# Kernel tuning notes

Measured on AMD Instinct MI355X. Metric: run time of the kernel, lower is better.

Reference implementation:

```python
import jax, jax.numpy as jnp
import numpy as np

EPS = 1e-4
TAU = 0.1
GAMMA = 64.0
RADIUS = 1.0
N_HEADS = 4
N_SPLIT = 4


def _l2norm(x, axis=-1):
    return x / jnp.maximum(jnp.linalg.norm(x, axis=axis, keepdims=True), 1e-12)


def _pd2(a, b):
    # pairwise squared distances: (B,N,M)
    return (jnp.sum(a * a, -1)[:, :, None] + jnp.sum(b * b, -1)[:, None, :]
            - 2.0 * jnp.einsum('bnd,bmd->bnm', a, b))


def _sim_matrix(xyz, nf, radius, gamma):
    # radius-masked Gaussian feature affinity, zero diagonal
    N = xyz.shape[1]
    d2x = _pd2(xyz, xyz)
    d2f = _pd2(nf, nf)
    A = jnp.exp(-gamma * d2f / nf.shape[-1]) * (d2x < radius * radius).astype(nf.dtype)
    return A * (1.0 - jnp.eye(N, dtype=A.dtype))


def _norm_lap(A, eps):
    deg = A.sum(-1)
    dinv = jax.lax.rsqrt(deg + eps)
    na = A * dinv[:, :, None] * dinv[:, None, :]
    lap = jnp.eye(A.shape[1], dtype=A.dtype) - na
    return lap, na


def _mincut(X, na, W1, b1, W2, b2, tau):
    # one GCN layer + temperature softmax soft assignment; pooled = weighted mean
    h = jax.nn.relu(jnp.einsum('bnm,bmc->bnc', na, X) @ W1 + b1)
    s = jax.nn.softmax((h @ W2 + b2) / tau, axis=-1)  # (B,N,K)
    denom = s.sum(1)[:, :, None] + EPS                # (B,K,1)
    c_fea = jnp.einsum('bnk,bnc->bkc', s, X) / denom
    return c_fea, s


def _centers(xyz, s):
    denom = s.sum(1)[:, :, None] + EPS
    return jnp.einsum('bnk,bnd->bkd', s, xyz) / denom


def _assignment_loss(p_xyz, c_xyz, s):
    d2 = _pd2(p_xyz, c_xyz)
    return jnp.mean(jnp.sum(s * d2, -1))


def _welsch(p_xyz, c_xyz, sigma):
    d2min = jnp.min(_pd2(p_xyz, c_xyz), -1)
    return jnp.mean(1.0 - jnp.exp(-d2min / (2.0 * sigma * sigma)))


def _knn_affinity(xyz, k):
    N = xyz.shape[1]
    d2 = _pd2(xyz, xyz)
    eye = jnp.eye(N, dtype=d2.dtype)
    neg = -(d2 + 1e6 * eye)
    thresh = jax.lax.top_k(neg, k)[0][..., -1:]
    mask = (neg >= thresh).astype(d2.dtype)
    A = jnp.exp(-d2) * mask * (1.0 - eye)
    return jnp.maximum(A, jnp.swapaxes(A, 1, 2))


def _cut_loss(na, xyz, alpha):
    N = xyz.shape[1]
    lap = jnp.eye(N, dtype=na.dtype) - na
    quad = jnp.einsum('bnd,bnm,bmd->b', xyz, lap, xyz)
    return alpha * jnp.mean(quad / N)


def _cross_attn(gf, cf, Wq, Wk, Wv, Wo, n_heads):
    B, N, C = gf.shape
    M = cf.shape[1]
    dh = C // n_heads
    q = (gf @ Wq).reshape(B, N, n_heads, dh)
    k = (cf @ Wk).reshape(B, M, n_heads, dh)
    v = (cf @ Wv).reshape(B, M, n_heads, dh)
    scores = jnp.einsum('bnhd,bmhd->bhnm', q, k) / np.sqrt(dh).astype(np.float32)
    attn = jax.nn.softmax(scores, -1)
    out = jnp.einsum('bhnm,bmhd->bnhd', attn, v).reshape(B, N, C) @ Wo
    return out, attn.mean(1)


def setup_inputs() -> dict:
    key = jax.random.key(0)
    ks = jax.random.split(key, 20)
    B, N_sp, C, H, K = 2, 1024, 256, 128, 64
    Kg = K // N_SPLIT
    sc = 1.0 / np.sqrt(C)
    sh = 1.0 / np.sqrt(H)
    return {
        'g_fea': jax.random.normal(ks[0], (B, N_sp, C), jnp.float32),
        'g_xyz': jax.random.uniform(ks[1], (B, N_sp, 3), jnp.float32),
        'p_fea_0': jax.random.normal(ks[2], (B, 4096, C), jnp.float32),
        'p_xyz_0': jax.random.uniform(ks[3], (B, 4096, 3), jnp.float32),
        'p_fea_1': jax.random.normal(ks[4], (B, 2048, C), jnp.float32),
        'p_xyz_1': jax.random.uniform(ks[5], (B, 2048, 3), jnp.float32),
        'lW1': jax.random.normal(ks[6], (C, H), jnp.float32) * sc,
        'lb1': jnp.zeros((H,), jnp.float32),
        'lW2': jax.random.normal(ks[7], (H, K), jnp.float32) * sh,
        'lb2': jnp.zeros((K,), jnp.float32),
        'gW1': jax.random.normal(ks[8], (C, H), jnp.float32) * sc,
        'gb1': jnp.zeros((H,), jnp.float32),
        'gW2': jax.random.normal(ks[9], (H, Kg), jnp.float32) * sh,
        'gb2': jnp.zeros((Kg,), jnp.float32),
        'Wq': jax.random.normal(ks[10], (C, C), jnp.float32) * sc,
        'Wk': jax.random.normal(ks[11], (C, C), jnp.float32) * sc,
        'Wv': jax.random.normal(ks[12], (C, C), jnp.float32) * sc,
        'Wo': jax.random.normal(ks[13], (C, C), jnp.float32) * sc,
    }


def reference(g_fea, g_xyz, p_fea_0, p_xyz_0, p_fea_1, p_xyz_1,
              lW1, lb1, lW2, lb2, gW1, gb1, gW2, gb2, Wq, Wk, Wv, Wo):
    l_loss = jnp.zeros((), jnp.float32)
    cx_list, cf_list = [], []
    for p_xyz_i, p_fea_i in ((p_xyz_0, p_fea_0), (p_xyz_1, p_fea_1)):
        nf = _l2norm(p_fea_i)
        A = _sim_matrix(p_xyz_i, nf, RADIUS, GAMMA)
        na = _norm_lap(A, EPS)[1]
        c_fea_i, s_i = _mincut(p_fea_i, na, lW1, lb1, lW2, lb2, TAU)
        c_xyz_i = _centers(p_xyz_i, s_i)
        c2p = jnp.einsum('bnk,bkc->bnc', s_i, jax.lax.stop_gradient(c_fea_i))
        l_loss = l_loss + _assignment_loss(p_xyz_i, c_xyz_i, s_i)
        l_loss = l_loss + jnp.linalg.norm(_l2norm(c2p) - nf) + _welsch(p_xyz_i, c_xyz_i, 1.0)
        cx_list.append(c_xyz_i)
        cf_list.append(c_fea_i)
    c_xyz = jnp.concatenate(cx_list, 1)
    c_fea = jnp.concatenate(cf_list, 1)
    A_c = _knn_affinity(c_xyz, 2 * N_SPLIT)
    na_c = _norm_lap(A_c, EPS)[1]
    c_fea_g, gs = _mincut(c_fea, na_c, gW1, gb1, gW2, gb2, TAU)
    c_xyz_g = _centers(c_xyz, gs)
    cut_loss_c = _assignment_loss(c_xyz, c_xyz_g, gs)
    agg, G_t = _cross_attn(g_fea, c_fea_g, Wq, Wk, Wv, Wo, N_HEADS)
    A_g = _sim_matrix(g_xyz, _l2norm(g_fea), 4.0 * RADIUS, GAMMA)
    ass_loss = _cut_loss(_norm_lap(A_g, EPS)[1], g_xyz, 1e-4)
    g_loss = jnp.mean(jnp.sum(jnp.linalg.norm(_l2norm(agg) - _l2norm(g_fea), axis=-1), 1)) + ass_loss
    return agg, l_loss + cut_loss_c, g_loss
```

## Files before the change

### kernel.cpp

```cpp
#include <hip/hip_runtime.h>

#define EPSF 1e-4f

typedef __attribute__((ext_vector_type(8))) short bf16x8;
typedef __attribute__((ext_vector_type(4))) float f32x4;

__device__ __forceinline__ unsigned short f2bf(float f){
    unsigned int u = __float_as_uint(f);
    return (unsigned short)((u + 0x7FFF + ((u >> 16) & 1)) >> 16);
}
__device__ __forceinline__ float bf2f(unsigned short u){
    return __uint_as_float(((unsigned int)u) << 16);
}
__device__ __forceinline__ float waveSum(float v){
    #pragma unroll
    for (int o = 32; o; o >>= 1) v += __shfl_xor(v, o, 64);
    return v;
}
__device__ __forceinline__ float waveMin(float v){
    #pragma unroll
    for (int o = 32; o; o >>= 1) v = fminf(v, __shfl_xor(v, o, 64));
    return v;
}
__device__ __forceinline__ float waveMax(float v){
    #pragma unroll
    for (int o = 32; o; o >>= 1) v = fmaxf(v, __shfl_xor(v, o, 64));
    return v;
}
__device__ __forceinline__ float blockReduceSum(float v, float* red, int nthr){
    int t = threadIdx.x;
    red[t] = v; __syncthreads();
    for (int s = nthr >> 1; s > 0; s >>= 1){
        if (t < s) red[t] += red[t + s];
        __syncthreads();
    }
    float r = red[0]; __syncthreads();
    return r;
}

__global__ void l2norm_kernel(const float* __restrict__ x, float* __restrict__ outf,
                              unsigned short* __restrict__ outb, int rows){
    __shared__ float red[256];
    int row = blockIdx.x, t = threadIdx.x;
    float v = x[(long)row*256 + t];
    float s = blockReduceSum(v*v, red, 256);
    float nrm = fmaxf(sqrtf(s), 1e-12f);
    float r = v / nrm;
    outf[(long)row*256 + t] = r;
    outb[(long)row*256 + t] = f2bf(r);
}

__global__ void cvt_bf16_kernel(const float* __restrict__ in, unsigned short* __restrict__ out, long n4){
    long i = (long)blockIdx.x*256 + threadIdx.x;
    if (i < n4){
        float4 v = ((const float4*)in)[i];
        unsigned int lo = f2bf(v.x) | ((unsigned int)f2bf(v.y) << 16);
        unsigned int hi = f2bf(v.z) | ((unsigned int)f2bf(v.w) << 16);
        uint2 u; u.x = lo; u.y = hi;
        ((uint2*)out)[i] = u;
    }
}

__global__ void tcvt_kernel(const float* __restrict__ W, unsigned short* __restrict__ WT,
                            int Rw, int Cw){
    __shared__ float tile[64][65];
    int r0 = blockIdx.x*64, c0 = blockIdx.y*64;
    int t = threadIdx.x;
    for (int idx = t; idx < 4096; idx += 256){
        int rr = idx >> 6, cc = idx & 63;
        tile[rr][cc] = (r0+rr < Rw && c0+cc < Cw) ? W[(long)(r0+rr)*Cw + c0+cc] : 0.f;
    }
    __syncthreads();
    for (int idx = t; idx < 4096; idx += 256){
        int cc = idx >> 6, rr = idx & 63;
        if (r0+rr < Rw && c0+cc < Cw)
            WT[(long)(c0+cc)*Rw + r0+rr] = f2bf(tile[rr][cc]);
    }
}

__global__ __launch_bounds__(256) void gram_mfma_kernel(const unsigned short* __restrict__ nf,
                                                        const float* __restrict__ xyz,
                                                        unsigned short* __restrict__ A,
                                                        float* __restrict__ deg,
                                                        int N, float r2, float scale){
    __shared__ short tA[128*32], tB[128*32];
    __shared__ float xa[384], xb[384];
    int tid = threadIdx.x;
    int n0 = blockIdx.y*128, m0 = blockIdx.x*128;
    for (int i = tid; i < 384; i += 256){ xa[i] = xyz[n0*3 + i]; xb[i] = xyz[m0*3 + i]; }
    int w = tid >> 6, l = tid & 63;
    int wy = w >> 1, wx = w & 1;
    int lg = l >> 4, lr = l & 15;
    int srow = tid >> 2, sc = tid & 3;
    f32x4 zero = {0.f, 0.f, 0.f, 0.f};
    f32x4 acc[4][4];
    #pragma unroll
    for (int i = 0; i < 4; ++i)
        #pragma unroll
        for (int j = 0; j < 4; ++j) acc[i][j] = zero;
    for (int kt = 0; kt < 256; kt += 32){
        __syncthreads();
        #pragma unroll
        for (int p = 0; p < 2; ++p){
            int row = srow + p*64;
            uint4 va = *(const uint4*)(nf + (long)(n0+row)*256 + kt + sc*8);
            uint4 vb = *(const uint4*)(nf + (long)(m0+row)*256 + kt + sc*8);
            *(uint4*)(tA + row*32 + sc*8) = va;
            *(uint4*)(tB + row*32 + sc*8) = vb;
        }
        __syncthreads();
        bf16x8 af[4], bfr[4];
        #pragma unroll
        for (int f = 0; f < 4; ++f){
            af[f]  = *(const bf16x8*)(tA + (wy*64 + f*16 + lr)*32 + lg*8);
            bfr[f] = *(const bf16x8*)(tB + (wx*64 + f*16 + lr)*32 + lg*8);
        }
        #pragma unroll
        for (int i = 0; i < 4; ++i)
            #pragma unroll
            for (int j = 0; j < 4; ++j)
                acc[i][j] = __builtin_amdgcn_mfma_f32_16x16x32_bf16(af[i], bfr[j], acc[i][j], 0, 0, 0);
    }
    #pragma unroll
    for (int fi = 0; fi < 4; ++fi){
        #pragma unroll
        for (int r = 0; r < 4; ++r){
            int n_ = wy*64 + fi*16 + lg*4 + r;
            int gn = n0 + n_;
            float rowacc = 0.f;
            #pragma unroll
            for (int fj = 0; fj < 4; ++fj){
                int m_ = wx*64 + fj*16 + lr;
                float dx = xa[n_*3+0]-xb[m_*3+0];
                float dy = xa[n_*3+1]-xb[m_*3+1];
                float dz = xa[n_*3+2]-xb[m_*3+2];
                float d2x = dx*dx + dy*dy + dz*dz;
                int gm = m0 + m_;
                float dot = acc[fi][fj][r];
                float val = (d2x < r2 && gn != gm) ? expf(scale*(2.f*dot - 2.f)) : 0.f;
                A[(long)gn*N + gm] = f2bf(val);
                rowacc += val;
            }
            rowacc += __shfl_xor(rowacc, 1, 64);
            rowacc += __shfl_xor(rowacc, 2, 64);
            rowacc += __shfl_xor(rowacc, 4, 64);
            rowacc += __shfl_xor(rowacc, 8, 64);
            if (lr == 0) atomicAdd(&deg[gn], rowacc);
        }
    }
}

__global__ __launch_bounds__(256) void transpose_scale_kernel(const float* __restrict__ fea,
                                                              const float* __restrict__ deg,
                                                              unsigned short* __restrict__ feaT,
                                                              unsigned short* __restrict__ xsT, int N){
    __shared__ float tile[64][65];
    __shared__ float dl[64];
    int m0 = blockIdx.x*64, c0 = blockIdx.y*64;
    int t = threadIdx.x;
    int lr = t >> 2, lc = (t & 3)*16;
    #pragma unroll
    for (int j = 0; j < 4; ++j){
        float4 v = *(const float4*)(fea + (long)(m0+lr)*256 + c0 + lc + j*4);
        tile[lr][lc+j*4+0] = v.x; tile[lr][lc+j*4+1] = v.y;
        tile[lr][lc+j*4+2] = v.z; tile[lr][lc+j*4+3] = v.w;
    }
    if (t < 64) dl[t] = rsqrtf(deg[m0+t] + EPSF);
    __syncthreads();
    unsigned short vr[16] __attribute__((aligned(16)));
    unsigned short vs[16] __attribute__((aligned(16)));
    #pragma unroll
    for (int j = 0; j < 16; ++j){
        float raw = tile[lc+j][lr];
        vr[j] = f2bf(raw);
        vs[j] = f2bf(raw * dl[lc+j]);
    }
    long off = (long)(c0+lr)*N + m0 + lc;
    *(uint4*)(feaT + off)     = *(uint4*)&vr[0];
    *(uint4*)(feaT + off + 8) = *(uint4*)&vr[8];
    *(uint4*)(xsT + off)      = *(uint4*)&vs[0];
    *(uint4*)(xsT + off + 8)  = *(uint4*)&vs[8];
}

__global__ __launch_bounds__(256) void ax_mfma_kernel(const unsigned short* __restrict__ A,
                                                      const unsigned short* __restrict__ xsT,
                                                      float* __restrict__ PY, int N){
    __shared__ short tA[128*32], tB[128*32];
    int tid = threadIdx.x;
    int c0 = blockIdx.x*128, n0 = blockIdx.y*128;
    int half = blockIdx.z;
    int kbase = half*(N/2), kend = kbase + N/2;
    int w = tid >> 6, l = tid & 63;
    int wy = w >> 1, wx = w & 1;
    int lg = l >> 4, lr = l & 15;
    int srow = tid >> 2, sc = tid & 3;
    f32x4 zero = {0.f, 0.f, 0.f, 0.f};
    f32x4 acc[4][4];
    #pragma unroll
    for (int i = 0; i < 4; ++i)
        #pragma unroll
        for (int j = 0; j < 4; ++j) acc[i][j] = zero;
    for (int kt = kbase; kt < kend; kt += 32){
        __syncthreads();
        #pragma unroll
        for (int p = 0; p < 2; ++p){
            int row = srow + p*64;
            uint4 va = *(const uint4*)(A   + (long)(n0+row)*N + kt + sc*8);
            uint4 vb = *(const uint4*)(xsT + (long)(c0+row)*N + kt + sc*8);
            *(uint4*)(tA + row*32 + sc*8) = va;
            *(uint4*)(tB + row*32 + sc*8) = vb;
        }
        __syncthreads();
        bf16x8 af[4], bfr[4];
        #pragma unroll
        for (int f = 0; f < 4; ++f){
            af[f]  = *(const bf16x8*)(tA + (wy*64 + f*16 + lr)*32 + lg*8);
            bfr[f] = *(const bf16x8*)(tB + (wx*64 + f*16 + lr)*32 + lg*8);
        }
        #pragma unroll
        for (int i = 0; i < 4; ++i)
            #pragma unroll
            for (int j = 0; j < 4; ++j)
                acc[i][j] = __builtin_amdgcn_mfma_f32_16x16x32_bf16(af[i], bfr[j], acc[i][j], 0, 0, 0);
    }
    float* out = PY + (long)half*N*256;
    #pragma unroll
    for (int fi = 0; fi < 4; ++fi){
        #pragma unroll
        for (int fj = 0; fj < 4; ++fj){
            #pragma unroll
            for (int r = 0; r < 4; ++r){
                int n_ = n0 + wy*64 + fi*16 + lg*4 + r;
                int c_ = c0 + wx*64 + fj*16 + lr;
                out[(long)n_*256 + c_] = acc[fi][fj][r];
            }
        }
    }
}

__global__ void combine_kernel(const float* __restrict__ PY, const float* __restrict__ deg,
                               unsigned short* __restrict__ Yb, int N){
    long i = (long)blockIdx.x*256 + threadIdx.x;
    long e = i*8;
    const float4* p0 = (const float4*)(PY + e);
    const float4* p1 = (const float4*)(PY + (long)N*256 + e);
    float4 a0 = p0[0], a1 = p0[1], b0 = p1[0], b1 = p1[1];
    float d = rsqrtf(deg[e >> 8] + EPSF);
    unsigned short vb[8] __attribute__((aligned(16)));
    vb[0] = f2bf((a0.x+b0.x)*d); vb[1] = f2bf((a0.y+b0.y)*d);
    vb[2] = f2bf((a0.z+b0.z)*d); vb[3] = f2bf((a0.w+b0.w)*d);
    vb[4] = f2bf((a1.x+b1.x)*d); vb[5] = f2bf((a1.y+b1.y)*d);
    vb[6] = f2bf((a1.z+b1.z)*d); vb[7] = f2bf((a1.w+b1.w)*d);
    *(uint4*)(Yb + e) = *(uint4*)vb;
}

__global__ __launch_bounds__(256) void gemm_XW_mfma_kernel(const unsigned short* __restrict__ X,
                                                           const unsigned short* __restrict__ WT,
                                                           const float* __restrict__ bias,
                                                           float* __restrict__ outF,
                                                           unsigned short* __restrict__ outB,
                                                           int R, int Ci, int Co, int relu){
    __shared__ short tA[128*32], tB[128*32];
    int tid = threadIdx.x;
    int c0 = blockIdx.x*128, r0 = blockIdx.y*128;
    int w = tid >> 6, l = tid & 63;
    int wy = w >> 1, wx = w & 1;
    int lg = l >> 4, lr = l & 15;
    int srow = tid >> 2, sc = tid & 3;
    f32x4 zero = {0.f, 0.f, 0.f, 0.f};
    f32x4 acc[4][4];
    #pragma unroll
    for (int i = 0; i < 4; ++i)
        #pragma unroll
        for (int j = 0; j < 4; ++j) acc[i][j] = zero;
    for (int kt = 0; kt < Ci; kt += 32){
        __syncthreads();
        #pragma unroll
        for (int p = 0; p < 2; ++p){
            int row = srow + p*64;
            uint4 va = {0,0,0,0}, vb = {0,0,0,0};
            int ar = r0 + row, br = c0 + row;
            if (ar < R)  va = *(const uint4*)(X  + (long)ar*Ci + kt + sc*8);
            if (br < Co) vb = *(const uint4*)(WT + (long)br*Ci + kt + sc*8);
            *(uint4*)(tA + row*32 + sc*8) = va;
            *(uint4*)(tB + row*32 + sc*8) = vb;
        }
        __syncthreads();
        bf16x8 af[4], bfr[4];
        #pragma unroll
        for (int f = 0; f < 4; ++f){
            af[f]  = *(const bf16x8*)(tA + (wy*64 + f*16 + lr)*32 + lg*8);
            bfr[f] = *(const bf16x8*)(tB + (wx*64 + f*16 + lr)*32 + lg*8);
        }
        #pragma unroll
        for (int i = 0; i < 4; ++i)
            #pragma unroll
            for (int j = 0; j < 4; ++j)
                acc[i][j] = __builtin_amdgcn_mfma_f32_16x16x32_bf16(af[i], bfr[j], acc[i][j], 0, 0, 0);
    }
    #pragma unroll
    for (int fi = 0; fi < 4; ++fi){
        #pragma unroll
        for (int fj = 0; fj < 4; ++fj){
            #pragma unroll
            for (int r = 0; r < 4; ++r){
                int rr = r0 + wy*64 + fi*16 + lg*4 + r;
                int cc = c0 + wx*64 + fj*16 + lr;
                if (rr < R && cc < Co){
                    float v = acc[fi][fj][r] + (bias ? bias[cc] : 0.f);
                    if (relu) v = fmaxf(v, 0.f);
                    if (outF) outF[(long)rr*Co + cc] = v;
                    if (outB) outB[(long)rr*Co + cc] = f2bf(v);
                }
            }
        }
    }
}

__global__ __launch_bounds__(256) void gemm_splitk_kernel(const float* __restrict__ X,
                                                          const float* __restrict__ W0,
                                                          const float* __restrict__ W1,
                                                          float* __restrict__ part,
                                                          int R, int Ci, int Co, int Ks){
    __shared__ float sa[32][65], sb[32][65];
    int tid = threadIdx.x, tx = tid & 15, ty = tid >> 4;
    int c0 = blockIdx.x * 64, r0 = blockIdx.y * 64;
    int z = blockIdx.z;
    const float* W = (z / Ks) ? W1 : W0;
    int kchunk = Ci / Ks, kst = (z % Ks) * kchunk;
    float acc[4][4] = {};
    for (int kt = kst; kt < kst + kchunk; kt += 32){
        #pragma unroll
        for (int p = 0; p < 8; ++p){
            int idx = p*256 + tid;
            int k = idx & 31, i = idx >> 5;
            int rr = r0 + i;
            sa[k][i] = (rr < R) ? X[(long)rr*Ci + kt + k] : 0.f;
            int j = idx & 63, kk = idx >> 6;
            int cc = c0 + j;
            sb[kk][j] = (cc < Co) ? W[(long)(kt+kk)*Co + cc] : 0.f;
        }
        __syncthreads();
        #pragma unroll
        for (int k = 0; k < 32; ++k){
            float a0=sa[k][ty*4+0],a1=sa[k][ty*4+1],a2=sa[k][ty*4+2],a3=sa[k][ty*4+3];
            float b0=sb[k][tx*4+0],b1=sb[k][tx*4+1],b2=sb[k][tx*4+2],b3=sb[k][tx*4+3];
            acc[0][0]+=a0*b0; acc[0][1]+=a0*b1; acc[0][2]+=a0*b2; acc[0][3]+=a0*b3;
            acc[1][0]+=a1*b0; acc[1][1]+=a1*b1; acc[1][2]+=a1*b2; acc[1][3]+=a1*b3;
            acc[2][0]+=a2*b0; acc[2][1]+=a2*b1; acc[2][2]+=a2*b2; acc[2][3]+=a2*b3;
            acc[3][0]+=a3*b0; acc[3][1]+=a3*b1; acc[3][2]+=a3*b2; acc[3][3]+=a3*b3;
        }
        __syncthreads();
    }
    float* outp = part + (long)z*R*Co;
    #pragma unroll
    for (int r = 0; r < 4; ++r){
        #pragma unroll
        for (int c = 0; c < 4; ++c){
            int rr = r0 + ty*4 + r, cc = c0 + tx*4 + c;
            if (rr < R && cc < Co) outp[(long)rr*Co + cc] = acc[r][c];
        }
    }
}

__global__ void combine_bias_kernel(const float* __restrict__ part, const float* __restrict__ bias,
                                    float* __restrict__ out, int R, int Co, int Ks, int relu){
    long i = (long)blockIdx.x*256 + threadIdx.x;
    if (i < (long)R*Co){
        long zs = (long)R*Co;
        float s = 0.f;
        for (int q = 0; q < Ks; ++q) s += part[q*zs + i];
        float v = s + (bias ? bias[i % Co] : 0.f);
        if (relu) v = fmaxf(v, 0.f);
        out[i] = v;
    }
}

__global__ __launch_bounds__(256) void softmaxT_kernel(float* __restrict__ s,
                                                       unsigned short* __restrict__ sT,
                                                       int sStride, float invtau){
    __shared__ unsigned short st[64][65];
    int blk = blockIdx.x, t = threadIdx.x, w = t >> 6, l = t & 63;
    #pragma unroll
    for (int i = 0; i < 16; ++i){
        int rloc = w + 4*i;
        long row = (long)blk*64 + rloc;
        float v = s[row*64 + l] * invtau;
        float mx = waveMax(v);
        float e = expf(v - mx);
        float sum = waveSum(e);
        float p = e / sum;
        s[row*64 + l] = p;
        st[l][rloc] = f2bf(p);
    }
    __syncthreads();
    int k = t >> 2, j = (t & 3)*16;
    unsigned short vbuf[16] __attribute__((aligned(16)));
    #pragma unroll
    for (int q = 0; q < 16; ++q) vbuf[q] = st[k][j+q];
    long off = (long)k*sStride + (long)blk*64 + j;
    *(uint4*)(sT + off)     = *(uint4*)&vbuf[0];
    *(uint4*)(sT + off + 8) = *(uint4*)&vbuf[8];
}

__global__ __launch_bounds__(256) void stx_mfma_kernel(const unsigned short* __restrict__ sT,
                                                       const unsigned short* __restrict__ feaT,
                                                       float* __restrict__ part,
                                                       int N, int split, int sStride){
    __shared__ short tA[64*32], tB[256*32];
    int tid = threadIdx.x;
    int z = blockIdx.x, b = z / split, chunk = z % split;
    int L = N / split, kst = chunk * L;
    const unsigned short* sTb = sT + (long)b*N;
    const unsigned short* fT  = feaT + (long)b*256*N;
    int w = tid >> 6, l = tid & 63;
    int lg = l >> 4, lr = l & 15;
    f32x4 zero = {0.f, 0.f, 0.f, 0.f};
    f32x4 acc[4][4];
    #pragma unroll
    for (int i = 0; i < 4; ++i)
        #pragma unroll
        for (int j = 0; j < 4; ++j) acc[i][j] = zero;
    int srow = tid >> 2, koff = (tid & 3)*8;
    for (int kt = kst; kt < kst + L; kt += 32){
        __syncthreads();
        *(uint4*)(tA + srow*32 + koff) = *(const uint4*)(sTb + (long)srow*sStride + kt + koff);
        #pragma unroll
        for (int p = 0; p < 4; ++p){
            int row = srow + p*64;
            *(uint4*)(tB + row*32 + koff) = *(const uint4*)(fT + (long)row*N + kt + koff);
        }
        __syncthreads();
        bf16x8 af[4], bfr[4];
        #pragma unroll
        for (int f = 0; f < 4; ++f){
            af[f]  = *(const bf16x8*)(tA + (f*16 + lr)*32 + lg*8);
            bfr[f] = *(const bf16x8*)(tB + (w*64 + f*16 + lr)*32 + lg*8);
        }
        #pragma unroll
        for (int i = 0; i < 4; ++i)
            #pragma unroll
            for (int j = 0; j < 4; ++j)
                acc[i][j] = __builtin_amdgcn_mfma_f32_16x16x32_bf16(af[i], bfr[j], acc[i][j], 0, 0, 0);
    }
    float* outp = part + (long)z*64*256;
    #pragma unroll
    for (int fi = 0; fi < 4; ++fi){
        #pragma unroll
        for (int fj = 0; fj < 4; ++fj){
            #pragma unroll
            for (int r = 0; r < 4; ++r){
                int kc = fi*16 + lg*4 + r;
                int cc = w*64 + fj*16 + lr;
                outp[(long)kc*256 + cc] = acc[fi][fj][r];
            }
        }
    }
}

__global__ void softmax_kernel(float* __restrict__ x, int Kc, float tau){
    int row = blockIdx.x, lane = threadIdx.x;
    bool act = lane < Kc;
    float v = act ? x[(long)row*Kc + lane] / tau : -1e30f;
    float mx = v;
    #pragma unroll
    for (int o = 32; o; o >>= 1) mx = fmaxf(mx, __shfl_xor(mx, o, 64));
    float e = act ? expf(v - mx) : 0.f;
    float s = e;
    #pragma unroll
    for (int o = 32; o; o >>= 1) s += __shfl_xor(s, o, 64);
    if (act) x[(long)row*Kc + lane] = e / s;
}

__global__ void cluster_xyz_kernel(const float* __restrict__ s, const float* __restrict__ xyz,
                                   float* __restrict__ outx, float* __restrict__ outd,
                                   int N, int Kc, int xBS, int dBS){
    __shared__ float red[256];
    int b = blockIdx.y, k = blockIdx.x, t = threadIdx.x;
    s   += (long)b*N*Kc;
    xyz += (long)b*N*3;
    float a0=0,a1=0,a2=0,ad=0;
    for (int n = t; n < N; n += 256){
        float sv = s[(long)n*Kc + k];
        ad += sv;
        a0 += sv*xyz[n*3+0]; a1 += sv*xyz[n*3+1]; a2 += sv*xyz[n*3+2];
    }
    a0 = blockReduceSum(a0, red, 256);
    a1 = blockReduceSum(a1, red, 256);
    a2 = blockReduceSum(a2, red, 256);
    ad = blockReduceSum(ad, red, 256);
    if (t == 0){
        outx[b*xBS + k*3+0] = a0;
        outx[b*xBS + k*3+1] = a1;
        outx[b*xBS + k*3+2] = a2;
        outd[b*dBS + k] = ad;
    }
}

__global__ __launch_bounds__(256) void gemm_sTX_kernel(const float* __restrict__ s,
                                                       const float* __restrict__ X,
                                                       float* __restrict__ part,
                                                       int N, int Kc, int split,
                                                       long sBS, long xBS){
    __shared__ float sa[32][65], sb[32][65];
    int tid = threadIdx.x, tx = tid & 15, ty = tid >> 4;
    int c0 = blockIdx.x * 64;
    int b = blockIdx.z / split, chunk = blockIdx.z % split;
    int L = N / split, nst = chunk * L;
    s += b*sBS; X += b*xBS;
    float* out = part + (long)blockIdx.z * Kc * 256;
    float acc[4][4] = {};
    for (int nt = nst; nt < nst + L; nt += 32){
        #pragma unroll
        for (int p = 0; p < 8; ++p){
            int idx = p*256 + tid;
            int i = idx & 63, k = idx >> 6;
            sa[k][i] = (i < Kc) ? s[(long)(nt+k)*Kc + i] : 0.f;
            int j = idx & 63, kk = idx >> 6;
            sb[kk][j] = X[(long)(nt+kk)*256 + c0 + j];
        }
        __syncthreads();
        #pragma unroll
        for (int k = 0; k < 32; ++k){
            float a0=sa[k][ty*4+0],a1=sa[k][ty*4+1],a2=sa[k][ty*4+2],a3=sa[k][ty*4+3];
            float b0=sb[k][tx*4+0],b1=sb[k][tx*4+1],b2=sb[k][tx*4+2],b3=sb[k][tx*4+3];
            acc[0][0]+=a0*b0; acc[0][1]+=a0*b1; acc[0][2]+=a0*b2; acc[0][3]+=a0*b3;
            acc[1][0]+=a1*b0; acc[1][1]+=a1*b1; acc[1][2]+=a1*b2; acc[1][3]+=a1*b3;
            acc[2][0]+=a2*b0; acc[2][1]+=a2*b1; acc[2][2]+=a2*b2; acc[2][3]+=a2*b3;
            acc[3][0]+=a3*b0; acc[3][1]+=a3*b1; acc[3][2]+=a3*b2; acc[3][3]+=a3*b3;
        }
        __syncthreads();
    }
    #pragma unroll
    for (int r = 0; r < 4; ++r){
        int kc = ty*4 + r;
        if (kc < Kc){
            #pragma unroll
            for (int c = 0; c < 4; ++c)
                out[(long)kc*256 + c0 + tx*4 + c] = acc[r][c];
        }
    }
}

__global__ void divide_sum_kernel(const float* __restrict__ part, const float* __restrict__ den,
                                  float* __restrict__ cfea, float* __restrict__ cxyz,
                                  int Kc, int split, int fBS, int xBS, int dBS){
    int b = blockIdx.y, k = blockIdx.x, t = threadIdx.x;
    float d = den[b*dBS + k] + EPSF;
    float s = 0.f;
    for (int q = 0; q < split; ++q)
        s += part[((long)(b*split+q)*Kc + k)*256 + t];
    cfea[(long)b*fBS + k*256 + t] = s / d;
    if (t < 3) cxyz[b*xBS + k*3 + t] /= d;
}

__global__ __launch_bounds__(256) void level_loss_kernel(const float* __restrict__ s,
                                                         const float* __restrict__ pxyz,
                                                         const float* __restrict__ cxyz,
                                                         const float* __restrict__ cfea,
                                                         const float* __restrict__ nf,
                                                         float* __restrict__ scal,
                                                         int N, float inv, int ndsSlot){
    __shared__ float cx[192];
    __shared__ float partA[4], partN[4];
    int b = blockIdx.y, t = threadIdx.x, w = t >> 6, l = t & 63;
    s    += (long)b*N*64;
    pxyz += (long)b*N*3;
    nf   += (long)b*N*256;
    cxyz += (long)b*384;
    cfea += (long)b*32768;
    if (t < 192) cx[t] = cxyz[t];
    __syncthreads();
    int n = blockIdx.x*4 + w;
    float sl = s[(long)n*64 + l];
    float px = pxyz[n*3+0], py = pxyz[n*3+1], pz = pxyz[n*3+2];
    float dx = px - cx[l*3+0], dy = py - cx[l*3+1], dz = pz - cx[l*3+2];
    float d2 = dx*dx + dy*dy + dz*dz;
    float assSum = waveSum(sl*d2);
    float dmin = waveMin(d2);
    float c0=0,c1=0,c2=0,c3=0;
    #pragma unroll 8
    for (int k = 0; k < 64; ++k){
        float sk = __shfl(sl, k, 64);
        const float* row = cfea + k*256;
        c0 += sk*row[l]; c1 += sk*row[l+64]; c2 += sk*row[l+128]; c3 += sk*row[l+192];
    }
    float nrm2 = waveSum(c0*c0 + c1*c1 + c2*c2 + c3*c3);
    float inrm = 1.f / fmaxf(sqrtf(nrm2), 1e-12f);
    const float* nfr = nf + (long)n*256;
    float e0 = c0*inrm - nfr[l];
    float e1 = c1*inrm - nfr[l+64];
    float e2 = c2*inrm - nfr[l+128];
    float e3 = c3*inrm - nfr[l+192];
    float nds = waveSum(e0*e0 + e1*e1 + e2*e2 + e3*e3);
    if (l == 0){
        partA[w] = inv*(assSum + 1.f - expf(-0.5f*dmin));
        partN[w] = nds;
    }
    __syncthreads();
    if (t == 0){
        int slot = blockIdx.x & 63;
        atomicAdd(&scal[slot], partA[0]+partA[1]+partA[2]+partA[3]);
        atomicAdd(&scal[ndsSlot*64 + slot], partN[0]+partN[1]+partN[2]+partN[3]);
    }
}

__global__ __launch_bounds__(128) void knn_nac_kernel(const float* __restrict__ cxyz,
                                                      float* __restrict__ nac){
    __shared__ float d2s[128][129];
    __shared__ float x[128][3];
    __shared__ float di[128];
    int b = blockIdx.x, n = threadIdx.x;
    x[n][0] = cxyz[b*384 + n*3+0];
    x[n][1] = cxyz[b*384 + n*3+1];
    x[n][2] = cxyz[b*384 + n*3+2];
    __syncthreads();
    float xn0 = x[n][0], xn1 = x[n][1], xn2 = x[n][2];
    for (int m = 0; m < 128; ++m){
        float dx = xn0-x[m][0], dy = xn1-x[m][1], dz = xn2-x[m][2];
        d2s[n][m] = dx*dx+dy*dy+dz*dz + (m==n ? 1e6f : 0.f);
    }
    float last = -1.f;
    for (int p = 0; p < 8; ++p){
        float cur = 1e30f;
        for (int m = 0; m < 128; ++m){
            float v = d2s[n][m];
            if (v > last && v < cur) cur = v;
        }
        last = cur;
    }
    for (int m = 0; m < 128; ++m){
        float d2 = d2s[n][m];
        d2s[n][m] = (m != n && d2 <= last) ? expf(-d2) : 0.f;
    }
    __syncthreads();
    for (int m = 0; m < 128; ++m){
        float v = fmaxf(d2s[n][m], d2s[m][n]);
        d2s[n][m] = v;
    }
    __syncthreads();
    float deg = 0.f;
    for (int m = 0; m < 128; ++m) deg += d2s[n][m];
    di[n] = rsqrtf(deg + EPSF);
    __syncthreads();
    float* Ab = nac + (long)b*16384;
    for (int c = 0; c < 128; ++c)
        Ab[c*128 + n] = d2s[c][n] * di[c] * di[n];
}

__global__ void bmm_small_kernel(const float* __restrict__ nac, const float* __restrict__ cfea,
                                 float* __restrict__ Y2){
    __shared__ float row[128];
    int b = blockIdx.y, n = blockIdx.x, t = threadIdx.x;
    if (t < 128) row[t] = nac[(long)b*16384 + n*128 + t];
    __syncthreads();
    float acc = 0.f;
    #pragma unroll 4
    for (int k = 0; k < 128; ++k) acc += row[k]*cfea[(long)b*32768 + k*256 + t];
    Y2[(long)b*32768 + n*256 + t] = acc;
}

__global__ void cutc_kernel(const float* __restrict__ gs, const float* __restrict__ cxyz,
                            const float* __restrict__ cxyzg, float* __restrict__ scal, float inv){
    __shared__ float cg[48];
    __shared__ float red[128];
    int b = blockIdx.x, t = threadIdx.x;
    if (t < 48) cg[t] = cxyzg[b*48 + t];
    __syncthreads();
    float x0 = cxyz[b*384 + t*3+0], x1 = cxyz[b*384 + t*3+1], x2 = cxyz[b*384 + t*3+2];
    float acc = 0.f;
    #pragma unroll
    for (int k = 0; k < 16; ++k){
        float dx = x0-cg[k*3+0], dy = x1-cg[k*3+1], dz = x2-cg[k*3+2];
        acc += gs[b*2048 + t*16 + k]*(dx*dx+dy*dy+dz*dz);
    }
    acc = blockReduceSum(acc, red, 128);
    if (t == 0) atomicAdd(&scal[b], acc*inv);
}

__global__ __launch_bounds__(256) void attn_kernel(const float* __restrict__ q,
                                                   const float* __restrict__ kk,
                                                   const float* __restrict__ vv,
                                                   unsigned short* __restrict__ aob){
    __shared__ float Ks[16][256], Vs[16][256];
    int b = blockIdx.y, n = blockIdx.x, t = threadIdx.x;
    #pragma unroll
    for (int p = 0; p < 16; ++p){
        int j = p*256 + t;
        Ks[j>>8][j&255] = kk[b*4096 + j];
        Vs[j>>8][j&255] = vv[b*4096 + j];
    }
    __syncthreads();
    float qv = q[((long)b*1024 + n)*256 + t];
    float sc[16];
    #pragma unroll
    for (int m = 0; m < 16; ++m){
        float v = qv * Ks[m][t];
        #pragma unroll
        for (int o = 32; o; o >>= 1) v += __shfl_xor(v, o, 64);
        sc[m] = v * 0.125f;
    }
    float mx = -1e30f;
    #pragma unroll
    for (int m = 0; m < 16; ++m) mx = fmaxf(mx, sc[m]);
    float sum = 0.f;
    #pragma unroll
    for (int m = 0; m < 16; ++m){ sc[m] = expf(sc[m]-mx); sum += sc[m]; }
    float o = 0.f;
    #pragma unroll
    for (int m = 0; m < 16; ++m) o += sc[m]*Vs[m][t];
    aob[((long)b*1024 + n)*256 + t] = f2bf(o / sum);
}

__global__ void quad_kernel(const unsigned short* __restrict__ A, const float* __restrict__ deg,
                            const float* __restrict__ xyz, float* __restrict__ scal){
    __shared__ float part[4];
    int t = threadIdx.x, w = t >> 6, l = t & 63;
    int n = blockIdx.x*4 + w;
    float a0=0,a1=0,a2=0;
    #pragma unroll 4
    for (int i = 0; i < 16; ++i){
        int m = l + i*64;
        float wv = bf2f(A[(long)n*1024 + m])*rsqrtf(deg[m] + EPSF);
        a0 += wv*xyz[m*3+0]; a1 += wv*xyz[m*3+1]; a2 += wv*xyz[m*3+2];
    }
    a0 = waveSum(a0); a1 = waveSum(a1); a2 = waveSum(a2);
    if (l == 0){
        float x0 = xyz[n*3+0], x1 = xyz[n*3+1], x2 = xyz[n*3+2];
        float dn = rsqrtf(deg[n] + EPSF);
        part[w] = (x0*x0+x1*x1+x2*x2) - dn*(x0*a0+x1*a1+x2*a2);
    }
    __syncthreads();
    if (t == 0) atomicAdd(&scal[4*64 + (blockIdx.x & 63)], part[0]+part[1]+part[2]+part[3]);
}

__global__ void gloss_kernel(const float* __restrict__ agg, const float* __restrict__ gfea,
                             float* __restrict__ scal){
    __shared__ float part[4];
    int t = threadIdx.x, w = t >> 6, l = t & 63;
    long r = (long)blockIdx.x*4 + w;
    const float* a = agg + r*256;
    const float* g = gfea + r*256;
    float a0=a[l],a1=a[l+64],a2=a[l+128],a3=a[l+192];
    float g0=g[l],g1=g[l+64],g2=g[l+128],g3=g[l+192];
    float na2 = waveSum(a0*a0+a1*a1+a2*a2+a3*a3);
    float ng2 = waveSum(g0*g0+g1*g1+g2*g2+g3*g3);
    float ia = 1.f/fmaxf(sqrtf(na2), 1e-12f), ig = 1.f/fmaxf(sqrtf(ng2), 1e-12f);
    float e0=a0*ia-g0*ig, e1=a1*ia-g1*ig, e2=a2*ia-g2*ig, e3=a3*ia-g3*ig;
    float d2 = waveSum(e0*e0+e1*e1+e2*e2+e3*e3);
    if (l == 0) part[w] = sqrtf(d2);
    __syncthreads();
    if (t == 0) atomicAdd(&scal[3*64 + (blockIdx.x & 63)], part[0]+part[1]+part[2]+part[3]);
}

__global__ void finalize_kernel(const float* __restrict__ scal, float* __restrict__ out){
    int t = threadIdx.x;
    float s[5];
    #pragma unroll
    for (int q = 0; q < 5; ++q){
        float v = scal[q*64 + t];
        #pragma unroll
        for (int o = 32; o; o >>= 1) v += __shfl_xor(v, o, 64);
        s[q] = v;
    }
    if (t == 0){
        out[524288] = s[0] + sqrtf(s[1]) + sqrtf(s[2]);
        out[524289] = s[3]*0.5f + 1e-4f*s[4]/2048.0f;
    }
}

extern "C" void kernel_launch(void* const* d_in, const int* in_sizes, int n_in,
                              void* d_out, int out_size, void* d_ws, size_t ws_size,
                              hipStream_t stream){
    const float* g_fea   = (const float*)d_in[0];
    const float* g_xyz   = (const float*)d_in[1];
    const float* p_fea_0 = (const float*)d_in[2];
    const float* p_xyz_0 = (const float*)d_in[3];
    const float* p_fea_1 = (const float*)d_in[4];
    const float* p_xyz_1 = (const float*)d_in[5];
    const float* lW1 = (const float*)d_in[6];
    const float* lb1 = (const float*)d_in[7];
    const float* lW2 = (const float*)d_in[8];
    const float* lb2 = (const float*)d_in[9];
    const float* gW1 = (const float*)d_in[10];
    const float* gb1 = (const float*)d_in[11];
    const float* gW2 = (const float*)d_in[12];
    const float* gb2 = (const float*)d_in[13];
    const float* Wq = (const float*)d_in[14];
    const float* Wk = (const float*)d_in[15];
    const float* Wv = (const float*)d_in[16];
    const float* Wo = (const float*)d_in[17];
    float* out = (float*)d_out;
    float* ws_f = (float*)d_ws;

    constexpr long O_SCALS = 0;
    constexpr long O_DEG   = O_SCALS + 512;
    constexpr long O_CFEA  = 16384;
    constexpr long O_CXYZ  = O_CFEA + 65536;
    constexpr long O_DEN   = O_CXYZ + 768;
    constexpr long O_CFG   = O_DEN  + 256;
    constexpr long O_CXG   = O_CFG  + 8192;
    constexpr long O_DENG  = O_CXG  + 96;
    constexpr long O_PART  = O_DENG + 64;
    constexpr long O_NF    = O_PART + 524288;
    constexpr long O_NFB   = O_NF   + 2097152;
    constexpr long O_XST   = O_NFB  + 1048576;
    constexpr long O_FEAT  = O_XST  + 1048576;
    constexpr long O_YB    = O_FEAT + 1048576;
    constexpr long O_HB    = O_YB   + 1048576;
    constexpr long O_S     = O_HB   + 524288;
    constexpr long O_ST    = O_S    + 524288;
    constexpr long O_PY    = O_ST   + 262144;
    constexpr long O_A     = O_PY   + 2097152;
    constexpr long O_Q     = O_A    + 8388608;
    constexpr long O_GFB   = O_Q    + 524288;
    constexpr long O_AOB   = O_GFB  + 262144;
    constexpr long O_KK    = O_AOB  + 262144;
    constexpr long O_VV    = O_KK   + 8192;
    constexpr long O_NAC   = O_VV   + 8192;
    constexpr long O_Y2    = O_NAC  + 32768;
    constexpr long O_H2    = O_Y2   + 65536;
    constexpr long O_LG2   = O_H2   + 32768;
    constexpr long O_W1T   = O_LG2  + 4096;
    constexpr long O_W2T   = O_W1T  + 16384;
    constexpr long O_WQT   = O_W2T  + 4096;
    constexpr long O_WOT   = O_WQT  + 32768;

    hipMemsetAsync(ws_f + O_SCALS, 0, (512 + 14336)*sizeof(float), stream);

    float* nf   = ws_f + O_NF;
    unsigned short* nfb  = (unsigned short*)(ws_f + O_NFB);
    unsigned short* xsT  = (unsigned short*)(ws_f + O_XST);
    unsigned short* feaT = (unsigned short*)(ws_f + O_FEAT);
    unsigned short* Ybb  = (unsigned short*)(ws_f + O_YB);
    unsigned short* Hb   = (unsigned short*)(ws_f + O_HB);
    unsigned short* sTb  = (unsigned short*)(ws_f + O_ST);
    unsigned short* A    = (unsigned short*)(ws_f + O_A);
    unsigned short* gfb  = (unsigned short*)(ws_f + O_GFB);
    unsigned short* aob  = (unsigned short*)(ws_f + O_AOB);
    unsigned short* lW1T = (unsigned short*)(ws_f + O_W1T);
    unsigned short* lW2T = (unsigned short*)(ws_f + O_W2T);
    unsigned short* WqT  = (unsigned short*)(ws_f + O_WQT);
    unsigned short* WoT  = (unsigned short*)(ws_f + O_WOT);
    float* sb   = ws_f + O_S;
    float* degA = ws_f + O_DEG;
    float* PY   = ws_f + O_PY;
    float* part = ws_f + O_PART;
    float* Qf   = ws_f + O_Q;

    tcvt_kernel<<<dim3(4, 2), 256, 0, stream>>>(lW1, lW1T, 256, 128);
    tcvt_kernel<<<dim3(2, 1), 256, 0, stream>>>(lW2, lW2T, 128, 64);
    tcvt_kernel<<<dim3(4, 4), 256, 0, stream>>>(Wq, WqT, 256, 256);
    tcvt_kernel<<<dim3(4, 4), 256, 0, stream>>>(Wo, WoT, 256, 256);
    cvt_bf16_kernel<<<512, 256, 0, stream>>>(g_fea, gfb, 131072);

    struct Lvl { const float* fea; const float* xyz; int N; int k0; int ndsSlot; long degBase; };
    Lvl lv[2] = {{p_fea_0, p_xyz_0, 4096, 0, 1, 0}, {p_fea_1, p_xyz_1, 2048, 64, 2, 8192}};

    for (int L = 0; L < 2; ++L){
        int N = lv[L].N;
        const float* fea = lv[L].fea;
        const float* xyz = lv[L].xyz;
        l2norm_kernel<<<2*N, 256, 0, stream>>>(fea, nf, nfb, 2*N);
        for (int b = 0; b < 2; ++b){
            float* degb = degA + lv[L].degBase + (long)b*N;
            gram_mfma_kernel<<<dim3(N/128, N/128), 256, 0, stream>>>(nfb + (long)b*N*256,
                                                                     xyz + (long)b*N*3, A, degb,
                                                                     N, 1.0f, 0.25f);
            transpose_scale_kernel<<<dim3(N/64, 4), 256, 0, stream>>>(fea + (long)b*N*256, degb,
                                                                      feaT + (long)b*256*N,
                                                                      xsT + (long)b*256*N, N);
            ax_mfma_kernel<<<dim3(2, N/128, 2), 256, 0, stream>>>(A, xsT + (long)b*256*N, PY, N);
            combine_kernel<<<N/8, 256, 0, stream>>>(PY, degb, Ybb + (long)b*N*256, N);
        }
        gemm_XW_mfma_kernel<<<dim3(1, 2*N/128), 256, 0, stream>>>(Ybb, lW1T, lb1, nullptr, Hb,
                                                                  2*N, 256, 128, 1);
        gemm_XW_mfma_kernel<<<dim3(1, 2*N/128), 256, 0, stream>>>(Hb, lW2T, lb2, sb, nullptr,
                                                                  2*N, 128, 64, 0);
        softmaxT_kernel<<<2*N/64, 256, 0, stream>>>(sb, sTb, 2*N, 10.0f);
        cluster_xyz_kernel<<<dim3(64, 2), 256, 0, stream>>>(sb, xyz, ws_f + O_CXYZ + lv[L].k0*3,
                                                            ws_f + O_DEN + lv[L].k0, N, 64, 384, 128);
        stx_mfma_kernel<<<32, 256, 0, stream>>>(sTb, feaT, part, N, 16, 2*N);
        divide_sum_kernel<<<dim3(64, 2), 256, 0, stream>>>(part, ws_f + O_DEN + lv[L].k0,
                                                           ws_f + O_CFEA + lv[L].k0*256,
                                                           ws_f + O_CXYZ + lv[L].k0*3,
                                                           64, 16, 128*256, 384, 128);
        level_loss_kernel<<<dim3(N/4, 2), 256, 0, stream>>>(sb, xyz, ws_f + O_CXYZ + lv[L].k0*3,
                                                            ws_f + O_CFEA + lv[L].k0*256, nf,
                                                            ws_f + O_SCALS, N, 1.0f/(2.0f*N), lv[L].ndsSlot);
    }

    knn_nac_kernel<<<2, 128, 0, stream>>>(ws_f + O_CXYZ, ws_f + O_NAC);
    bmm_small_kernel<<<dim3(128, 2), 256, 0, stream>>>(ws_f + O_NAC, ws_f + O_CFEA, ws_f + O_Y2);
    gemm_splitk_kernel<<<dim3(2, 4, 4), 256, 0, stream>>>(ws_f + O_Y2, gW1, nullptr, part,
                                                          256, 256, 128, 4);
    combine_bias_kernel<<<128, 256, 0, stream>>>(part, gb1, ws_f + O_H2, 256, 128, 4, 1);
    gemm_splitk_kernel<<<dim3(1, 4, 4), 256, 0, stream>>>(ws_f + O_H2, gW2, nullptr, part,
                                                          256, 128, 16, 4);
    combine_bias_kernel<<<16, 256, 0, stream>>>(part, gb2, ws_f + O_LG2, 256, 16, 4, 0);
    softmax_kernel<<<256, 64, 0, stream>>>(ws_f + O_LG2, 16, 0.1f);
    cluster_xyz_kernel<<<dim3(16, 2), 256, 0, stream>>>(ws_f + O_LG2, ws_f + O_CXYZ,
                                                        ws_f + O_CXG, ws_f + O_DENG, 128, 16, 48, 16);
    gemm_sTX_kernel<<<dim3(4, 1, 8), 256, 0, stream>>>(ws_f + O_LG2, ws_f + O_CFEA, part,
                                                       128, 16, 4, 128L*16, 128L*256);
    divide_sum_kernel<<<dim3(16, 2), 256, 0, stream>>>(part, ws_f + O_DENG, ws_f + O_CFG,
                                                       ws_f + O_CXG, 16, 4, 16*256, 48, 16);
    cutc_kernel<<<2, 128, 0, stream>>>(ws_f + O_LG2, ws_f + O_CXYZ, ws_f + O_CXG,
                                       ws_f + O_SCALS, 1.0f/256.0f);

    gemm_XW_mfma_kernel<<<dim3(2, 16), 256, 0, stream>>>(gfb, WqT, nullptr, Qf, nullptr,
                                                         2048, 256, 256, 0);
    gemm_splitk_kernel<<<dim3(4, 1, 16), 256, 0, stream>>>(ws_f + O_CFG, Wk, Wv, part,
                                                           32, 256, 256, 8);
    combine_bias_kernel<<<32, 256, 0, stream>>>(part, nullptr, ws_f + O_KK, 32, 256, 8, 0);
    combine_bias_kernel<<<32, 256, 0, stream>>>(part + 8L*32*256, nullptr, ws_f + O_VV, 32, 256, 8, 0);
    attn_kernel<<<dim3(1024, 2), 256, 0, stream>>>(Qf, ws_f + O_KK, ws_f + O_VV, aob);
    gemm_XW_mfma_kernel<<<dim3(2, 16), 256, 0, stream>>>(aob, WoT, nullptr, out, nullptr,
                                                         2048, 256, 256, 0);

    l2norm_kernel<<<2048, 256, 0, stream>>>(g_fea, nf, nfb, 2048);
    for (int b = 0; b < 2; ++b){
        float* degb = degA + 12288 + (long)b*1024;
        gram_mfma_kernel<<<dim3(8, 8), 256, 0, stream>>>(nfb + (long)b*1024*256, g_xyz + (long)b*1024*3,
                                                         A, degb, 1024, 16.0f, 0.25f);
        quad_kernel<<<256, 256, 0, stream>>>(A, degb, g_xyz + (long)b*1024*3, ws_f + O_SCALS);
    }

    gloss_kernel<<<512, 256, 0, stream>>>(out, g_fea, ws_f + O_SCALS);
    finalize_kernel<<<1, 64, 0, stream>>>(ws_f + O_SCALS, out);
}
```

Measured before the change: 782.9 us.

## Increase split-K for adjacency GEMM, prefetch GEMM tiles, drop fp32 normalized features

Raises the split-K factor of the adjacency-times-features MFMA GEMM from 2 to 8 and generalizes the combine step to sum 8 partials, so small levels launch more blocks. Both MFMA GEMMs now prefetch the next K-tile into registers while computing the current one. The fp32 normalized-feature output is removed and the level loss reads the bf16 copy instead; that loss also stages cluster features in a 64KB shared buffer. The trade-offs are more partial-sum traffic, lower occupancy in the loss kernel and slightly lower precision in the loss term.

```diff
diff --git a/kernel.cpp b/kernel.cpp
--- a/kernel.cpp
+++ b/kernel.cpp
@@ -38,16 +38,13 @@
     return r;
 }
 
-__global__ void l2norm_kernel(const float* __restrict__ x, float* __restrict__ outf,
-                              unsigned short* __restrict__ outb, int rows){
+__global__ void l2norm_kernel(const float* __restrict__ x, unsigned short* __restrict__ outb, int rows){
     __shared__ float red[256];
     int row = blockIdx.x, t = threadIdx.x;
     float v = x[(long)row*256 + t];
     float s = blockReduceSum(v*v, red, 256);
     float nrm = fmaxf(sqrtf(s), 1e-12f);
-    float r = v / nrm;
-    outf[(long)row*256 + t] = r;
-    outb[(long)row*256 + t] = f2bf(r);
+    outb[(long)row*256 + t] = f2bf(v / nrm);
 }
 
 __global__ void cvt_bf16_kernel(const float* __restrict__ in, unsigned short* __restrict__ out, long n4){
@@ -184,12 +181,12 @@
 
 __global__ __launch_bounds__(256) void ax_mfma_kernel(const unsigned short* __restrict__ A,
                                                       const unsigned short* __restrict__ xsT,
-                                                      float* __restrict__ PY, int N){
+                                                      float* __restrict__ PY, int N, int split){
     __shared__ short tA[128*32], tB[128*32];
     int tid = threadIdx.x;
     int c0 = blockIdx.x*128, n0 = blockIdx.y*128;
-    int half = blockIdx.z;
-    int kbase = half*(N/2), kend = kbase + N/2;
+    int chunk = blockIdx.z;
+    int L = N/split, kbase = chunk*L, kend = kbase + L;
     int w = tid >> 6, l = tid & 63;
     int wy = w >> 1, wx = w & 1;
     int lg = l >> 4, lr = l & 15;
@@ -200,17 +197,30 @@
     for (int i = 0; i < 4; ++i)
         #pragma unroll
         for (int j = 0; j < 4; ++j) acc[i][j] = zero;
+    uint4 pva[2], pvb[2];
+    #pragma unroll
+    for (int p = 0; p < 2; ++p){
+        int row = srow + p*64;
+        pva[p] = *(const uint4*)(A   + (long)(n0+row)*N + kbase + sc*8);
+        pvb[p] = *(const uint4*)(xsT + (long)(c0+row)*N + kbase + sc*8);
+    }
     for (int kt = kbase; kt < kend; kt += 32){
         __syncthreads();
         #pragma unroll
         for (int p = 0; p < 2; ++p){
             int row = srow + p*64;
-            uint4 va = *(const uint4*)(A   + (long)(n0+row)*N + kt + sc*8);
-            uint4 vb = *(const uint4*)(xsT + (long)(c0+row)*N + kt + sc*8);
-            *(uint4*)(tA + row*32 + sc*8) = va;
-            *(uint4*)(tB + row*32 + sc*8) = vb;
-        }
-        __syncthreads();
+            *(uint4*)(tA + row*32 + sc*8) = pva[p];
+            *(uint4*)(tB + row*32 + sc*8) = pvb[p];
+        }
+        __syncthreads();
+        if (kt + 32 < kend){
+            #pragma unroll
+            for (int p = 0; p < 2; ++p){
+                int row = srow + p*64;
+                pva[p] = *(const uint4*)(A   + (long)(n0+row)*N + kt + 32 + sc*8);
+                pvb[p] = *(const uint4*)(xsT + (long)(c0+row)*N + kt + 32 + sc*8);
+            }
+        }
         bf16x8 af[4], bfr[4];
         #pragma unroll
         for (int f = 0; f < 4; ++f){
@@ -223,7 +233,7 @@
             for (int j = 0; j < 4; ++j)
                 acc[i][j] = __builtin_amdgcn_mfma_f32_16x16x32_bf16(af[i], bfr[j], acc[i][j], 0, 0, 0);
     }
-    float* out = PY + (long)half*N*256;
+    float* out = PY + (long)chunk*N*256;
     #pragma unroll
     for (int fi = 0; fi < 4; ++fi){
         #pragma unroll
@@ -239,18 +249,22 @@
 }
 
 __global__ void combine_kernel(const float* __restrict__ PY, const float* __restrict__ deg,
-                               unsigned short* __restrict__ Yb, int N){
+                               unsigned short* __restrict__ Yb, int N, int split){
     long i = (long)blockIdx.x*256 + threadIdx.x;
     long e = i*8;
-    const float4* p0 = (const float4*)(PY + e);
-    const float4* p1 = (const float4*)(PY + (long)N*256 + e);
-    float4 a0 = p0[0], a1 = p0[1], b0 = p1[0], b1 = p1[1];
+    float4 s0 = {0,0,0,0}, s1 = {0,0,0,0};
+    for (int q = 0; q < split; ++q){
+        const float4* p = (const float4*)(PY + (long)q*N*256 + e);
+        float4 a = p[0], b = p[1];
+        s0.x += a.x; s0.y += a.y; s0.z += a.z; s0.w += a.w;
+        s1.x += b.x; s1.y += b.y; s1.z += b.z; s1.w += b.w;
+    }
     float d = rsqrtf(deg[e >> 8] + EPSF);
     unsigned short vb[8] __attribute__((aligned(16)));
-    vb[0] = f2bf((a0.x+b0.x)*d); vb[1] = f2bf((a0.y+b0.y)*d);
-    vb[2] = f2bf((a0.z+b0.z)*d); vb[3] = f2bf((a0.w+b0.w)*d);
-    vb[4] = f2bf((a1.x+b1.x)*d); vb[5] = f2bf((a1.y+b1.y)*d);
-    vb[6] = f2bf((a1.z+b1.z)*d); vb[7] = f2bf((a1.w+b1.w)*d);
+    vb[0] = f2bf(s0.x*d); vb[1] = f2bf(s0.y*d);
+    vb[2] = f2bf(s0.z*d); vb[3] = f2bf(s0.w*d);
+    vb[4] = f2bf(s1.x*d); vb[5] = f2bf(s1.y*d);
+    vb[6] = f2bf(s1.z*d); vb[7] = f2bf(s1.w*d);
     *(uint4*)(Yb + e) = *(uint4*)vb;
 }
 
@@ -273,19 +287,32 @@
     for (int i = 0; i < 4; ++i)
         #pragma unroll
         for (int j = 0; j < 4; ++j) acc[i][j] = zero;
+    uint4 pva[2], pvb[2];
+    #pragma unroll
+    for (int p = 0; p < 2; ++p){
+        int row = srow + p*64;
+        int ar = r0 + row, br = c0 + row;
+        pva[p] = (ar < R)  ? *(const uint4*)(X  + (long)ar*Ci + sc*8) : (uint4){0,0,0,0};
+        pvb[p] = (br < Co) ? *(const uint4*)(WT + (long)br*Ci + sc*8) : (uint4){0,0,0,0};
+    }
     for (int kt = 0; kt < Ci; kt += 32){
         __syncthreads();
         #pragma unroll
         for (int p = 0; p < 2; ++p){
             int row = srow + p*64;
-            uint4 va = {0,0,0,0}, vb = {0,0,0,0};
-            int ar = r0 + row, br = c0 + row;
-            if (ar < R)  va = *(const uint4*)(X  + (long)ar*Ci + kt + sc*8);
-            if (br < Co) vb = *(const uint4*)(WT + (long)br*Ci + kt + sc*8);
-            *(uint4*)(tA + row*32 + sc*8) = va;
-            *(uint4*)(tB + row*32 + sc*8) = vb;
-        }
-        __syncthreads();
+            *(uint4*)(tA + row*32 + sc*8) = pva[p];
+            *(uint4*)(tB + row*32 + sc*8) = pvb[p];
+        }
+        __syncthreads();
+        if (kt + 32 < Ci){
+            #pragma unroll
+            for (int p = 0; p < 2; ++p){
+                int row = srow + p*64;
+                int ar = r0 + row, br = c0 + row;
+                pva[p] = (ar < R)  ? *(const uint4*)(X  + (long)ar*Ci + kt + 32 + sc*8) : (uint4){0,0,0,0};
+                pvb[p] = (br < Co) ? *(const uint4*)(WT + (long)br*Ci + kt + 32 + sc*8) : (uint4){0,0,0,0};
+            }
+        }
         bf16x8 af[4], bfr[4];
         #pragma unroll
         for (int f = 0; f < 4; ++f){
@@ -558,17 +585,20 @@
                                                          const float* __restrict__ pxyz,
                                                          const float* __restrict__ cxyz,
                                                          const float* __restrict__ cfea,
-                                                         const float* __restrict__ nf,
+                                                         const unsigned short* __restrict__ nfb,
                                                          float* __restrict__ scal,
                                                          int N, float inv, int ndsSlot){
+    __shared__ float cf[64*256];
     __shared__ float cx[192];
     __shared__ float partA[4], partN[4];
     int b = blockIdx.y, t = threadIdx.x, w = t >> 6, l = t & 63;
     s    += (long)b*N*64;
     pxyz += (long)b*N*3;
-    nf   += (long)b*N*256;
+    nfb  += (long)b*N*256;
     cxyz += (long)b*384;
     cfea += (long)b*32768;
+    for (int i = t; i < 4096; i += 256)
+        ((float4*)cf)[i] = ((const float4*)cfea)[i];
     if (t < 192) cx[t] = cxyz[t];
     __syncthreads();
     int n = blockIdx.x*4 + w;
@@ -582,16 +612,16 @@
     #pragma unroll 8
     for (int k = 0; k < 64; ++k){
         float sk = __shfl(sl, k, 64);
-        const float* row = cfea + k*256;
+        const float* row = cf + k*256;
         c0 += sk*row[l]; c1 += sk*row[l+64]; c2 += sk*row[l+128]; c3 += sk*row[l+192];
     }
     float nrm2 = waveSum(c0*c0 + c1*c1 + c2*c2 + c3*c3);
     float inrm = 1.f / fmaxf(sqrtf(nrm2), 1e-12f);
-    const float* nfr = nf + (long)n*256;
-    float e0 = c0*inrm - nfr[l];
-    float e1 = c1*inrm - nfr[l+64];
-    float e2 = c2*inrm - nfr[l+128];
-    float e3 = c3*inrm - nfr[l+192];
+    const unsigned short* nfr = nfb + (long)n*256;
+    float e0 = c0*inrm - bf2f(nfr[l]);
+    float e1 = c1*inrm - bf2f(nfr[l+64]);
+    float e2 = c2*inrm - bf2f(nfr[l+128]);
+    float e3 = c3*inrm - bf2f(nfr[l+192]);
     float nds = waveSum(e0*e0 + e1*e1 + e2*e2 + e3*e3);
     if (l == 0){
         partA[w] = inv*(assSum + 1.f - expf(-0.5f*dmin));
@@ -794,7 +824,7 @@
     float* ws_f = (float*)d_ws;
 
     constexpr long O_SCALS = 0;
-    constexpr long O_DEG   = O_SCALS + 512;
+    constexpr long O_DEG   = 512;
     constexpr long O_CFEA  = 16384;
     constexpr long O_CXYZ  = O_CFEA + 65536;
     constexpr long O_DEN   = O_CXYZ + 768;
@@ -802,8 +832,7 @@
     constexpr long O_CXG   = O_CFG  + 8192;
     constexpr long O_DENG  = O_CXG  + 96;
     constexpr long O_PART  = O_DENG + 64;
-    constexpr long O_NF    = O_PART + 524288;
-    constexpr long O_NFB   = O_NF   + 2097152;
+    constexpr long O_NFB   = O_PART + 524288;
     constexpr long O_XST   = O_NFB  + 1048576;
     constexpr long O_FEAT  = O_XST  + 1048576;
     constexpr long O_YB    = O_FEAT + 1048576;
@@ -811,7 +840,7 @@
     constexpr long O_S     = O_HB   + 524288;
     constexpr long O_ST    = O_S    + 524288;
     constexpr long O_PY    = O_ST   + 262144;
-    constexpr long O_A     = O_PY   + 2097152;
+    constexpr long O_A     = O_PY   + 8388608;
     constexpr long O_Q     = O_A    + 8388608;
     constexpr long O_GFB   = O_Q    + 524288;
     constexpr long O_AOB   = O_GFB  + 262144;
@@ -828,7 +857,6 @@
 
     hipMemsetAsync(ws_f + O_SCALS, 0, (512 + 14336)*sizeof(float), stream);
 
-    float* nf   = ws_f + O_NF;
     unsigned short* nfb  = (unsigned short*)(ws_f + O_NFB);
     unsigned short* xsT  = (unsigned short*)(ws_f + O_XST);
     unsigned short* feaT = (unsigned short*)(ws_f + O_FEAT);
@@ -861,7 +889,7 @@
         int N = lv[L].N;
         const float* fea = lv[L].fea;
         const float* xyz = lv[L].xyz;
-        l2norm_kernel<<<2*N, 256, 0, stream>>>(fea, nf, nfb, 2*N);
+        l2norm_kernel<<<2*N, 256, 0, stream>>>(fea, nfb, 2*N);
         for (int b = 0; b < 2; ++b){
             float* degb = degA + lv[L].degBase + (long)b*N;
             gram_mfma_kernel<<<dim3(N/128, N/128), 256, 0, stream>>>(nfb + (long)b*N*256,
@@ -870,8 +898,8 @@
             transpose_scale_kernel<<<dim3(N/64, 4), 256, 0, stream>>>(fea + (long)b*N*256, degb,
                                                                       feaT + (long)b*256*N,
                                                                       xsT + (long)b*256*N, N);
-            ax_mfma_kernel<<<dim3(2, N/128, 2), 256, 0, stream>>>(A, xsT + (long)b*256*N, PY, N);
-            combine_kernel<<<N/8, 256, 0, stream>>>(PY, degb, Ybb + (long)b*N*256, N);
+            ax_mfma_kernel<<<dim3(2, N/128, 8), 256, 0, stream>>>(A, xsT + (long)b*256*N, PY, N, 8);
+            combine_kernel<<<N/8, 256, 0, stream>>>(PY, degb, Ybb + (long)b*N*256, N, 8);
         }
         gemm_XW_mfma_kernel<<<dim3(1, 2*N/128), 256, 0, stream>>>(Ybb, lW1T, lb1, nullptr, Hb,
                                                                   2*N, 256, 128, 1);
@@ -886,7 +914,7 @@
                                                            ws_f + O_CXYZ + lv[L].k0*3,
                                                            64, 16, 128*256, 384, 128);
         level_loss_kernel<<<dim3(N/4, 2), 256, 0, stream>>>(sb, xyz, ws_f + O_CXYZ + lv[L].k0*3,
-                                                            ws_f + O_CFEA + lv[L].k0*256, nf,
+                                                            ws_f + O_CFEA + lv[L].k0*256, nfb,
                                                             ws_f + O_SCALS, N, 1.0f/(2.0f*N), lv[L].ndsSlot);
     }
 
@@ -918,7 +946,7 @@
     gemm_XW_mfma_kernel<<<dim3(2, 16), 256, 0, stream>>>(aob, WoT, nullptr, out, nullptr,
                                                          2048, 256, 256, 0);
 
-    l2norm_kernel<<<2048, 256, 0, stream>>>(g_fea, nf, nfb, 2048);
+    l2norm_kernel<<<2048, 256, 0, stream>>>(g_fea, nfb, 2048);
     for (int b = 0; b < 2; ++b){
         float* degb = degA + 12288 + (long)b*1024;
         gram_mfma_kernel<<<dim3(8, 8), 256, 0, stream>>>(nfb + (long)b*1024*256, g_xyz + (long)b*1024*3,
```

Result: no change. 770.0 us (-1.6%).
